# Performance work log

Hardware: AMD Instinct MI355X
Metric: run time of the kernel (lower is better)

The kernel has to match this reference:

```python
import jax, jax.numpy as jnp
import numpy as np

T, J, IC = 243, 17, 32
C = J * IC            # 544 embed dim
BS = 3                # block_size
NB = T // BS          # 81 num_blocks
K = 6                 # top_k
H = 8                 # num_heads
DEPTH = 2
HID = int(C * 2.0)    # 1088 mlp hidden
EPS = 1e-6


def _ln(x, g, b):
    m = x.mean(-1, keepdims=True)
    v = ((x - m) ** 2).mean(-1, keepdims=True)
    return (x - m) * jax.lax.rsqrt(v + EPS) * g + b


def setup_inputs() -> dict:
    key = jax.random.key(0)
    ks = jax.random.split(key, 16)
    s = 0.02
    B = 512
    return {
        "x": jax.random.normal(ks[0], (B, T, J, IC), jnp.float32),
        "pos_embed": s * jax.random.normal(ks[1], (1, T, C), jnp.float32),
        "fc1_w": s * jax.random.normal(ks[2], (NB, NB), jnp.float32),
        "fc2_w": s * jax.random.normal(ks[3], (NB, NB), jnp.float32),
        "ln1_g": jnp.ones((DEPTH, C), jnp.float32),
        "ln1_b": jnp.zeros((DEPTH, C), jnp.float32),
        "qkv_w": s * jax.random.normal(ks[4], (DEPTH, 3 * C, C), jnp.float32),
        "qkv_b": jnp.zeros((DEPTH, 3 * C), jnp.float32),
        "proj_w": s * jax.random.normal(ks[5], (DEPTH, C, C), jnp.float32),
        "proj_b": jnp.zeros((DEPTH, C), jnp.float32),
        "ln2_g": jnp.ones((DEPTH, C), jnp.float32),
        "ln2_b": jnp.zeros((DEPTH, C), jnp.float32),
        "mfc1_w": s * jax.random.normal(ks[6], (DEPTH, HID, C), jnp.float32),
        "mfc1_b": jnp.zeros((DEPTH, HID), jnp.float32),
        "mfc2_w": s * jax.random.normal(ks[7], (DEPTH, C, HID), jnp.float32),
        "mfc2_b": jnp.zeros((DEPTH, C), jnp.float32),
        "lnf_g": jnp.ones((C,), jnp.float32),
        "lnf_b": jnp.zeros((C,), jnp.float32),
        "wm2_w": s * jax.random.normal(ks[8], (K,), jnp.float32),
        "wm2_b": jnp.zeros((1,), jnp.float32),
    }


def reference(x, pos_embed, fc1_w, fc2_w, ln1_g, ln1_b, qkv_w, qkv_b,
              proj_w, proj_b, ln2_g, ln2_b, mfc1_w, mfc1_b, mfc2_w, mfc2_b,
              lnf_g, lnf_b, wm2_w, wm2_b):
    B = x.shape[0]
    x = x.reshape(B, T, C) + pos_embed                       # [B,T,C]
    # time_shift: zero-pad one frame at the front, keep first T rows, first C/2 chans
    shifted = jnp.pad(x, ((0, 0), (1, 0), (0, 0)))[:, :T, :C // 2]
    x = jnp.concatenate([shifted, x[:, :, C // 2:]], axis=2)
    # block pooling
    xb = x.reshape(B, NB, BS, C).mean(axis=2)                # [B,NB,C]
    # BlockAttention: global avg over C -> gated MLP -> topk -> gather
    y = xb.mean(axis=2)                                      # [B,NB]
    y = jax.nn.sigmoid(jnp.maximum(y @ fc1_w.T, 0.0) @ fc2_w.T)
    _, idx = jax.lax.top_k(y, K)                             # [B,K]
    t = jnp.take_along_axis(xb, idx[:, :, None], axis=1)     # [B,K,C]
    scale = (C // H) ** -0.5
    for i in range(DEPTH):
        h = _ln(t, ln1_g[i], ln1_b[i])
        qkv = (h @ qkv_w[i].T + qkv_b[i]).reshape(B, K, 3, H, C // H)
        q, k, v = qkv[:, :, 0], qkv[:, :, 1], qkv[:, :, 2]   # [B,K,H,hd]
        attn = jax.nn.softmax(jnp.einsum('bnhd,bmhd->bhnm', q, k) * scale, axis=-1)
        o = jnp.einsum('bhnm,bmhd->bnhd', attn, v).reshape(B, K, C)
        t = t + o @ proj_w[i].T + proj_b[i]
        h = _ln(t, ln2_g[i], ln2_b[i])
        h = jax.nn.gelu(h @ mfc1_w[i].T + mfc1_b[i], approximate=False)
        t = t + (h @ mfc2_w[i].T + mfc2_b[i])
    t = _ln(t, lnf_g, lnf_b)
    out = jnp.einsum('bkc,k->bc', t, wm2_w) + wm2_b          # Conv1d(K,1,ks=1)
    return out.reshape(B, 1, J, C // J)
```

## Files before the change

kernel.cpp:

```cpp
#include <hip/hip_runtime.h>
#include <hip/hip_bf16.h>
#include <math.h>

#define TT 243
#define CC 544
#define NBB 81
#define KK 6
#define HH 8
#define HD 68
#define DEPTH 2
#define HID 1088
#define BB 512
#define MTOK 3072
#define EPSF 1e-6f

typedef __attribute__((ext_vector_type(8))) short bf16x8;
typedef __attribute__((ext_vector_type(4))) float f32x4;

__device__ __forceinline__ __hip_bfloat16 f2b(float f) { return __float2bfloat16(f); }
__device__ __forceinline__ unsigned short f2bu(float f) {
    __hip_bfloat16 h = __float2bfloat16(f);
    return *(unsigned short*)&h;
}
__device__ __forceinline__ float b2f_lo(unsigned int u) { return __uint_as_float(u << 16); }
__device__ __forceinline__ float b2f_hi(unsigned int u) { return __uint_as_float(u & 0xffff0000u); }

#define E0 443904
#define E1 591872
#define E2 887808
#define E3 1183744

#define RS_BLOCKS 3888
#define PS_BLOCKS 8
#define WC_BLOCKS 4624
#define BW_GRID (RS_BLOCKS + PS_BLOCKS + WC_BLOCKS)

__global__ __launch_bounds__(256, 4) void bw_kernel(
    const float* __restrict__ x,
    const float* __restrict__ pos,
    const float* __restrict__ qkvw, const float* __restrict__ projw,
    const float* __restrict__ mfc1w, const float* __restrict__ mfc2w,
    unsigned short* __restrict__ wbf,
    float* __restrict__ L,
    float* __restrict__ R,
    float* __restrict__ pLR)
{
    const int blk = blockIdx.x;
    const int tid = threadIdx.x;

    if (blk < RS_BLOCKS) {
        const int w = tid >> 6;
        const int lane = tid & 63;
        const int oct = lane & 7;
        const int rsub = lane >> 3;
        const int r = (blk * 4 + w) * 8 + rsub;
        const float4* xr = (const float4*)x + (size_t)r * 136;
        float4 xs[17];
#pragma unroll
        for (int j = 0; j < 17; ++j) xs[j] = xr[oct + j * 8];
        float aL = 0.0f, aR = 0.0f;
#pragma unroll
        for (int j = 0; j < 17; ++j) {
            const float s = (xs[j].x + xs[j].y) + (xs[j].z + xs[j].w);
            if (j < 8) aL += s;
            else if (j == 8) { if (oct < 4) aL += s; else aR += s; }
            else aR += s;
        }
#pragma unroll
        for (int m = 1; m < 8; m <<= 1) {
            aL += __shfl_xor(aL, m);
            aR += __shfl_xor(aR, m);
        }
        if (oct == 0) { L[r] = aL; R[r] = aR; }
        return;
    }

    if (blk < RS_BLOCKS + PS_BLOCKS) {
        const int w = tid >> 6;
        const int lane = tid & 63;
        const int oct = lane & 7;
        const int rsub = lane >> 3;
        const int r = (blk - RS_BLOCKS) * 32 + w * 8 + rsub;
        const int rc = (r < TT) ? r : (TT - 1);
        const float4* pr = (const float4*)pos + (size_t)rc * 136;
        float4 xs[17];
#pragma unroll
        for (int j = 0; j < 17; ++j) xs[j] = pr[oct + j * 8];
        float aL = 0.0f, aR = 0.0f;
#pragma unroll
        for (int j = 0; j < 17; ++j) {
            const float s = (xs[j].x + xs[j].y) + (xs[j].z + xs[j].w);
            if (j < 8) aL += s;
            else if (j == 8) { if (oct < 4) aL += s; else aR += s; }
            else aR += s;
        }
#pragma unroll
        for (int m = 1; m < 8; m <<= 1) {
            aL += __shfl_xor(aL, m);
            aR += __shfl_xor(aR, m);
        }
        if (oct == 0 && r < TT) { pLR[r] = aL; pLR[TT + r] = aR; }
        return;
    }

    const int i = (blk - RS_BLOCKS - PS_BLOCKS) * 256 + tid;
    if (i < E3) {
        float4 v;
        if (i < E0)      v = ((const float4*)qkvw)[i];
        else if (i < E1) v = ((const float4*)projw)[i - E0];
        else if (i < E2) v = ((const float4*)mfc1w)[i - E1];
        else             v = ((const float4*)mfc2w)[i - E2];
        ushort4 o;
        o.x = f2bu(v.x); o.y = f2bu(v.y); o.z = f2bu(v.z); o.w = f2bu(v.w);
        ((ushort4*)wbf)[i] = o;
    }
}

__global__ __launch_bounds__(128) void select_kernel(
    const float* __restrict__ L, const float* __restrict__ R,
    const float* __restrict__ pLR,
    const float* __restrict__ fc1, const float* __restrict__ fc2,
    const float* __restrict__ x, const float* __restrict__ pos,
    const float* __restrict__ ln1g, const float* __restrict__ ln1b,
    float* __restrict__ t,
    unsigned short* __restrict__ hb)
{
    const int b = blockIdx.x;
    const int tid = threadIdx.x;
    __shared__ float sf1[NBB * NBB];
    __shared__ float sf2[NBB * NBB];
    __shared__ float sy[NBB], sz[NBB], swv[NBB];
    __shared__ int sidx[KK];
    __shared__ __align__(16) float st[KK][CC];

    const int w = tid >> 6;
    const int lane = tid & 63;
    const float4* x4 = (const float4*)x;
    const float4* p4 = (const float4*)pos;

    for (int i = tid; i < NBB * NBB; i += 128) {
        sf1[i] = fc1[i];
        sf2[i] = fc2[i];
    }

    if (tid < NBB) {
        const int n = tid;
        const float* Lb = L + (size_t)b * TT;
        const float* Rb = R + (size_t)b * TT;
        const float* pL = pLR;
        const float* pR = pLR + TT;
        float s = Lb[3 * n] + Lb[3 * n + 1] + Rb[3 * n] + Rb[3 * n + 1] + Rb[3 * n + 2]
                + pL[3 * n] + pL[3 * n + 1] + pR[3 * n] + pR[3 * n + 1] + pR[3 * n + 2];
        if (n > 0) s += Lb[3 * n - 1] + pL[3 * n - 1];
        sy[n] = s * (1.0f / (3.0f * (float)CC));
    }
    __syncthreads();
    if (tid < NBB) {
        float s = 0.0f;
        for (int j = 0; j < NBB; ++j) s += sf1[tid * NBB + j] * sy[j];
        sz[tid] = fmaxf(s, 0.0f);
    }
    __syncthreads();
    if (tid < NBB) {
        float s = 0.0f;
        for (int j = 0; j < NBB; ++j) s += sf2[tid * NBB + j] * sz[j];
        swv[tid] = 1.0f / (1.0f + expf(-s));
    }
    __syncthreads();
    if (w == 0) {
        float va = (lane < NBB) ? swv[lane] : -1e30f;
        float vb = (lane + 64 < NBB) ? swv[lane + 64] : -1e30f;
        const int ia = lane, ib = lane + 64;
        for (int kk = 0; kk < KK; ++kk) {
            float v = va; int idx = ia;
            if (vb > v) { v = vb; idx = ib; }
#pragma unroll
            for (int m = 1; m < 64; m <<= 1) {
                const float ov = __shfl_xor(v, m);
                const int oi = __shfl_xor(idx, m);
                if (ov > v || (ov == v && oi < idx)) { v = ov; idx = oi; }
            }
            if (lane == 0) sidx[kk] = idx;
            if (ia == idx) va = -1e30f;
            if (ib == idx) vb = -1e30f;
        }
    }
    __syncthreads();

    for (int i = tid; i < KK * 136; i += 128) {
        const int k = i / 136;
        const int c4 = i - k * 136;
        const int n = sidx[k];
        const int shift = (c4 < 68) ? -1 : 0;
        float ax = 0.f, ay = 0.f, az = 0.f, aw = 0.f;
#pragma unroll
        for (int i2 = 0; i2 < 3; ++i2) {
            const int ttr = 3 * n + i2 + shift;
            if (ttr >= 0) {
                const float4 xv = x4[((size_t)b * TT + ttr) * 136 + c4];
                const float4 pv = p4[(size_t)ttr * 136 + c4];
                ax += xv.x + pv.x; ay += xv.y + pv.y; az += xv.z + pv.z; aw += xv.w + pv.w;
            }
        }
        const float inv3 = 1.0f / 3.0f;
        const float4 a = make_float4(ax * inv3, ay * inv3, az * inv3, aw * inv3);
        *(float4*)&st[k][c4 * 4] = a;
        ((float4*)t)[((size_t)b * KK + k) * 136 + c4] = a;
    }
    __syncthreads();

    for (int k = w; k < KK; k += 2) {
        float s = 0.0f, s2 = 0.0f;
        for (int c = lane; c < CC; c += 64) { const float v = st[k][c]; s += v; s2 += v * v; }
#pragma unroll
        for (int off = 32; off; off >>= 1) {
            s += __shfl_xor(s, off);
            s2 += __shfl_xor(s2, off);
        }
        const float m = s / (float)CC;
        const float inv = rsqrtf(s2 / (float)CC - m * m + EPSF);
        for (int c4 = lane; c4 < 136; c4 += 64) {
            const float4 v = *(const float4*)&st[k][c4 * 4];
            const float4 gv = ((const float4*)ln1g)[c4];
            const float4 bv = ((const float4*)ln1b)[c4];
            ushort4 o;
            o.x = f2bu((v.x - m) * inv * gv.x + bv.x);
            o.y = f2bu((v.y - m) * inv * gv.y + bv.y);
            o.z = f2bu((v.z - m) * inv * gv.z + bv.z);
            o.w = f2bu((v.w - m) * inv * gv.w + bv.w);
            ((ushort4*)hb)[((size_t)b * KK + k) * 136 + c4] = o;
        }
    }
}

__global__ __launch_bounds__(256) void ln_bf16_kernel(
    const float* __restrict__ X, const float* __restrict__ g,
    const float* __restrict__ bta, unsigned short* __restrict__ Y)
{
    const int row = blockIdx.x * 4 + (threadIdx.x >> 6);
    const int lane = threadIdx.x & 63;
    const float4* xr4 = (const float4*)(X + (size_t)row * CC);
    const float4 v0 = xr4[lane];
    const float4 v1 = xr4[lane + 64];
    float4 v2 = make_float4(0.f, 0.f, 0.f, 0.f);
    if (lane < 8) v2 = xr4[lane + 128];
    float s = (v0.x + v0.y + v0.z + v0.w) + (v1.x + v1.y + v1.z + v1.w)
            + (v2.x + v2.y + v2.z + v2.w);
    float s2 = (v0.x * v0.x + v0.y * v0.y + v0.z * v0.z + v0.w * v0.w)
             + (v1.x * v1.x + v1.y * v1.y + v1.z * v1.z + v1.w * v1.w)
             + (v2.x * v2.x + v2.y * v2.y + v2.z * v2.z + v2.w * v2.w);
#pragma unroll
    for (int off = 32; off; off >>= 1) {
        s += __shfl_xor(s, off);
        s2 += __shfl_xor(s2, off);
    }
    const float m = s / (float)CC;
    const float inv = rsqrtf(s2 / (float)CC - m * m + EPSF);
    ushort4* yr = (ushort4*)(Y + (size_t)row * CC);
    {
        const float4 gv = ((const float4*)g)[lane];
        const float4 bv = ((const float4*)bta)[lane];
        ushort4 o;
        o.x = f2bu((v0.x - m) * inv * gv.x + bv.x);
        o.y = f2bu((v0.y - m) * inv * gv.y + bv.y);
        o.z = f2bu((v0.z - m) * inv * gv.z + bv.z);
        o.w = f2bu((v0.w - m) * inv * gv.w + bv.w);
        yr[lane] = o;
    }
    {
        const float4 gv = ((const float4*)g)[lane + 64];
        const float4 bv = ((const float4*)bta)[lane + 64];
        ushort4 o;
        o.x = f2bu((v1.x - m) * inv * gv.x + bv.x);
        o.y = f2bu((v1.y - m) * inv * gv.y + bv.y);
        o.z = f2bu((v1.z - m) * inv * gv.z + bv.z);
        o.w = f2bu((v1.w - m) * inv * gv.w + bv.w);
        yr[lane + 64] = o;
    }
    if (lane < 8) {
        const float4 gv = ((const float4*)g)[lane + 128];
        const float4 bv = ((const float4*)bta)[lane + 128];
        ushort4 o;
        o.x = f2bu((v2.x - m) * inv * gv.x + bv.x);
        o.y = f2bu((v2.y - m) * inv * gv.y + bv.y);
        o.z = f2bu((v2.z - m) * inv * gv.z + bv.z);
        o.w = f2bu((v2.w - m) * inv * gv.w + bv.w);
        yr[lane + 128] = o;
    }
}

template <int ACT, int RES, int OBF>
__global__ __launch_bounds__(256) void gemm_mfma_kernel(
    const unsigned short* __restrict__ X,
    const unsigned short* __restrict__ W,
    const float* __restrict__ bias,
    const float* __restrict__ Rr,
    void* __restrict__ Y,
    int M, int N, int Kd)
{
    const int bm = blockIdx.y * 128;
    const int bn = blockIdx.x * 128;
    const int tid = threadIdx.x;
    const int K8 = Kd >> 3;

    __shared__ __align__(16) short As[128][72];
    __shared__ __align__(16) short Bs[128][72];

    const int r0 = tid >> 2;
    const int c0 = tid & 3;
    const int r1 = r0 + 64;

    const uint4* Xu = (const uint4*)X;
    const uint4* Wu = (const uint4*)W;

    const int wid = tid >> 6;
    const int lane = tid & 63;
    const int wm = (wid >> 1) * 64;
    const int wn = (wid & 1) * 64;
    const int l16 = lane & 15;
    const int l4 = lane >> 4;
    const int koff = l4 * 8;

    f32x4 acc[4][4] = {};

    const int wr0 = min(bn + r0, N - 1);
    const int wr1 = min(bn + r1, N - 1);

    const uint4 zz = {0u, 0u, 0u, 0u};
    uint4 a00, a01, a10, a11, b00, b01, b10, b11;
    {
        const int k1 = c0, k2 = c0 + 4;
        a00 = (k1 < K8) ? Xu[(size_t)(bm + r0) * K8 + k1] : zz;
        a01 = (k2 < K8) ? Xu[(size_t)(bm + r0) * K8 + k2] : zz;
        a10 = (k1 < K8) ? Xu[(size_t)(bm + r1) * K8 + k1] : zz;
        a11 = (k2 < K8) ? Xu[(size_t)(bm + r1) * K8 + k2] : zz;
        b00 = (k1 < K8) ? Wu[(size_t)wr0 * K8 + k1] : zz;
        b01 = (k2 < K8) ? Wu[(size_t)wr0 * K8 + k2] : zz;
        b10 = (k1 < K8) ? Wu[(size_t)wr1 * K8 + k1] : zz;
        b11 = (k2 < K8) ? Wu[(size_t)wr1 * K8 + k2] : zz;
    }

    const int nk = (Kd + 63) >> 6;
    for (int kt = 0; kt < nk; ++kt) {
        __syncthreads();
        *(uint4*)&As[r0][c0 * 8]       = a00;
        *(uint4*)&As[r0][(c0 + 4) * 8] = a01;
        *(uint4*)&As[r1][c0 * 8]       = a10;
        *(uint4*)&As[r1][(c0 + 4) * 8] = a11;
        *(uint4*)&Bs[r0][c0 * 8]       = b00;
        *(uint4*)&Bs[r0][(c0 + 4) * 8] = b01;
        *(uint4*)&Bs[r1][c0 * 8]       = b10;
        *(uint4*)&Bs[r1][(c0 + 4) * 8] = b11;
        __syncthreads();

        if (kt + 1 < nk) {
            const int k1 = (kt + 1) * 8 + c0;
            const int k2 = k1 + 4;
            a00 = (k1 < K8) ? Xu[(size_t)(bm + r0) * K8 + k1] : zz;
            a01 = (k2 < K8) ? Xu[(size_t)(bm + r0) * K8 + k2] : zz;
            a10 = (k1 < K8) ? Xu[(size_t)(bm + r1) * K8 + k1] : zz;
            a11 = (k2 < K8) ? Xu[(size_t)(bm + r1) * K8 + k2] : zz;
            b00 = (k1 < K8) ? Wu[(size_t)wr0 * K8 + k1] : zz;
            b01 = (k2 < K8) ? Wu[(size_t)wr0 * K8 + k2] : zz;
            b10 = (k1 < K8) ? Wu[(size_t)wr1 * K8 + k1] : zz;
            b11 = (k2 < K8) ? Wu[(size_t)wr1 * K8 + k2] : zz;
        }

#pragma unroll
        for (int kh = 0; kh < 2; ++kh) {
            bf16x8 af[4], bf[4];
#pragma unroll
            for (int mf = 0; mf < 4; ++mf)
                af[mf] = *(const bf16x8*)&As[wm + mf * 16 + l16][kh * 32 + koff];
#pragma unroll
            for (int nf = 0; nf < 4; ++nf)
                bf[nf] = *(const bf16x8*)&Bs[wn + nf * 16 + l16][kh * 32 + koff];
#pragma unroll
            for (int mf = 0; mf < 4; ++mf)
#pragma unroll
                for (int nf = 0; nf < 4; ++nf)
                    acc[mf][nf] = __builtin_amdgcn_mfma_f32_16x16x32_bf16(af[mf], bf[nf], acc[mf][nf], 0, 0, 0);
        }
    }

#pragma unroll
    for (int nf = 0; nf < 4; ++nf) {
        const int col = bn + wn + nf * 16 + l16;
        if (col < N) {
            const float bs = bias[col];
#pragma unroll
            for (int mf = 0; mf < 4; ++mf) {
#pragma unroll
                for (int j = 0; j < 4; ++j) {
                    const int row = bm + wm + mf * 16 + l4 * 4 + j;
                    float v = acc[mf][nf][j] + bs;
                    if (ACT == 1) v = 0.5f * v * (1.0f + erff(v * 0.70710678118654752f));
                    if (RES) v += Rr[(size_t)row * N + col];
                    if (OBF) ((unsigned short*)Y)[(size_t)row * N + col] = f2bu(v);
                    else     ((float*)Y)[(size_t)row * N + col] = v;
                }
            }
        }
    }
}

__global__ __launch_bounds__(512) void attn_kernel(
    const unsigned short* __restrict__ qkv,
    __hip_bfloat16* __restrict__ o)
{
    const int b = blockIdx.x;
    __shared__ __align__(16) float sq[KK * 3 * CC];
    __shared__ float sp[HH][40];
    const int tid = threadIdx.x;

    const uint4* src4 = (const uint4*)(qkv + (size_t)b * KK * 3 * CC);
    for (int i = tid; i < (KK * 3 * CC) / 8; i += 512) {
        const uint4 u = src4[i];
        float4 f0, f1;
        f0.x = b2f_lo(u.x); f0.y = b2f_hi(u.x);
        f0.z = b2f_lo(u.y); f0.w = b2f_hi(u.y);
        f1.x = b2f_lo(u.z); f1.y = b2f_hi(u.z);
        f1.z = b2f_lo(u.w); f1.w = b2f_hi(u.w);
        ((float4*)sq)[2 * i] = f0;
        ((float4*)sq)[2 * i + 1] = f1;
    }
    __syncthreads();

    const int h = tid >> 6;
    const int lane = tid & 63;
    const float scl = rsqrtf((float)HD);

    if (lane < KK * KK) {
        const int n = lane / KK, m = lane - (lane / KK) * KK;
        const float* qp = &sq[n * (3 * CC) + 0 * CC + h * HD];
        const float* kp = &sq[m * (3 * CC) + 1 * CC + h * HD];
        float s = 0.0f;
#pragma unroll 4
        for (int d = 0; d < HD; ++d) s += qp[d] * kp[d];
        sp[h][lane] = s * scl;
    }
    __syncthreads();
    if (lane < KK) {
        const int n = lane;
        float mx = -1e30f;
#pragma unroll
        for (int m = 0; m < KK; ++m) mx = fmaxf(mx, sp[h][n * KK + m]);
        float e[KK];
        float sum = 0.0f;
#pragma unroll
        for (int m = 0; m < KK; ++m) { e[m] = expf(sp[h][n * KK + m] - mx); sum += e[m]; }
        const float inv = 1.0f / sum;
#pragma unroll
        for (int m = 0; m < KK; ++m) sp[h][n * KK + m] = e[m] * inv;
    }
    __syncthreads();
    for (int i = tid; i < KK * CC; i += 512) {
        const int n = i / CC;
        const int cd = i - n * CC;
        const int hh = cd / HD;
        const int d = cd - hh * HD;
        float acc = 0.0f;
#pragma unroll
        for (int m = 0; m < KK; ++m)
            acc += sp[hh][n * KK + m] * sq[m * (3 * CC) + 2 * CC + hh * HD + d];
        o[(size_t)b * KK * CC + i] = f2b(acc);
    }
}

__global__ __launch_bounds__(256) void final_kernel(
    const float* __restrict__ t, const float* __restrict__ g,
    const float* __restrict__ bta, const float* __restrict__ wm2w,
    const float* __restrict__ wm2b, float* __restrict__ out)
{
    const int b = blockIdx.x;
    const int tid = threadIdx.x;
    __shared__ float st[KK][CC];
    __shared__ float sm[KK], si[KK];
    const float* tb = t + (size_t)b * KK * CC;
    for (int i = tid; i < KK * CC; i += 256) st[i / CC][i % CC] = tb[i];
    __syncthreads();
    const int wid = tid >> 6, lane = tid & 63;
    for (int r = wid; r < KK; r += 4) {
        float s = 0.0f, s2 = 0.0f;
        for (int c = lane; c < CC; c += 64) { const float v = st[r][c]; s += v; s2 += v * v; }
#pragma unroll
        for (int off = 32; off; off >>= 1) { s += __shfl_xor(s, off); s2 += __shfl_xor(s2, off); }
        if (lane == 0) {
            const float m = s / (float)CC;
            sm[r] = m;
            si[r] = rsqrtf(s2 / (float)CC - m * m + EPSF);
        }
    }
    __syncthreads();
    const float w0 = wm2w[0], w1 = wm2w[1], w2 = wm2w[2], w3 = wm2w[3], w4 = wm2w[4], w5 = wm2w[5];
    const float wb = wm2b[0];
    for (int c = tid; c < CC; c += 256) {
        const float gg = g[c], bb = bta[c];
        float acc = wb;
        acc += w0 * ((st[0][c] - sm[0]) * si[0] * gg + bb);
        acc += w1 * ((st[1][c] - sm[1]) * si[1] * gg + bb);
        acc += w2 * ((st[2][c] - sm[2]) * si[2] * gg + bb);
        acc += w3 * ((st[3][c] - sm[3]) * si[3] * gg + bb);
        acc += w4 * ((st[4][c] - sm[4]) * si[4] * gg + bb);
        acc += w5 * ((st[5][c] - sm[5]) * si[5] * gg + bb);
        out[(size_t)b * CC + c] = acc;
    }
}

extern "C" void kernel_launch(void* const* d_in, const int* in_sizes, int n_in,
                              void* d_out, int out_size, void* d_ws, size_t ws_size,
                              hipStream_t stream)
{
    const float* x      = (const float*)d_in[0];
    const float* pos    = (const float*)d_in[1];
    const float* fc1_w  = (const float*)d_in[2];
    const float* fc2_w  = (const float*)d_in[3];
    const float* ln1_g  = (const float*)d_in[4];
    const float* ln1_b  = (const float*)d_in[5];
    const float* qkv_w  = (const float*)d_in[6];
    const float* qkv_b  = (const float*)d_in[7];
    const float* proj_w = (const float*)d_in[8];
    const float* proj_b = (const float*)d_in[9];
    const float* ln2_g  = (const float*)d_in[10];
    const float* ln2_b  = (const float*)d_in[11];
    const float* mfc1_w = (const float*)d_in[12];
    const float* mfc1_b = (const float*)d_in[13];
    const float* mfc2_w = (const float*)d_in[14];
    const float* mfc2_b = (const float*)d_in[15];
    const float* lnf_g  = (const float*)d_in[16];
    const float* lnf_b  = (const float*)d_in[17];
    const float* wm2_w  = (const float*)d_in[18];
    const float* wm2_b  = (const float*)d_in[19];

    float* ws = (float*)d_ws;
    float* L    = ws;
    float* R    = L + 124416;
    float* pLR  = R + 124416;
    float* t    = pLR + 512;
    unsigned short* qkvb = (unsigned short*)(t + (size_t)MTOK * CC);
    unsigned short* hb  = qkvb + (size_t)MTOK * 3 * CC;
    unsigned short* ob  = hb + (size_t)MTOK * CC;
    unsigned short* gb  = ob + (size_t)MTOK * CC;
    unsigned short* wbf = gb + (size_t)MTOK * HID;

    unsigned short* wqkv = wbf;
    unsigned short* wprj = wbf + 1775616;
    unsigned short* wf1  = wbf + 2367488;
    unsigned short* wf2  = wbf + 3551232;

    bw_kernel<<<BW_GRID, 256, 0, stream>>>(
        x, pos, qkv_w, proj_w, mfc1_w, mfc2_w, wbf, L, R, pLR);

    select_kernel<<<BB, 128, 0, stream>>>(
        L, R, pLR, fc1_w, fc2_w, x, pos, ln1_g, ln1_b, t, hb);

    for (int i = 0; i < DEPTH; ++i) {
        if (i > 0) {
            ln_bf16_kernel<<<MTOK / 4, 256, 0, stream>>>(t, ln1_g + i * CC, ln1_b + i * CC, hb);
        }
        gemm_mfma_kernel<0, 0, 1><<<dim3(13, 24), 256, 0, stream>>>(
            hb, wqkv + (size_t)i * 1632 * 544, qkv_b + (size_t)i * 3 * CC,
            nullptr, qkvb, MTOK, 3 * CC, CC);
        attn_kernel<<<BB, 512, 0, stream>>>(qkvb, (__hip_bfloat16*)ob);
        gemm_mfma_kernel<0, 1, 0><<<dim3(5, 24), 256, 0, stream>>>(
            ob, wprj + (size_t)i * 544 * 544, proj_b + (size_t)i * CC,
            t, t, MTOK, CC, CC);
        ln_bf16_kernel<<<MTOK / 4, 256, 0, stream>>>(t, ln2_g + i * CC, ln2_b + i * CC, hb);
        gemm_mfma_kernel<1, 0, 1><<<dim3(9, 24), 256, 0, stream>>>(
            hb, wf1 + (size_t)i * HID * 544, mfc1_b + (size_t)i * HID,
            nullptr, gb, MTOK, HID, CC);
        gemm_mfma_kernel<0, 1, 0><<<dim3(5, 24), 256, 0, stream>>>(
            gb, wf2 + (size_t)i * 544 * HID, mfc2_b + (size_t)i * CC,
            t, t, MTOK, CC, HID);
    }

    final_kernel<<<BB, 256, 0, stream>>>(t, lnf_g, lnf_b, wm2_w, wm2_b, (float*)d_out);
}
```

Before: 253.2 us.

## Fuse LayerNorm into GEMMs via per-row partial statistics from residual epilogues

```diff
diff --git a/kernel.cpp b/kernel.cpp
--- a/kernel.cpp
+++ b/kernel.cpp
@@ -13,6 +13,7 @@
 #define BB 512
 #define MTOK 3072
 #define EPSF 1e-6f
+#define NPART 10
 
 typedef __attribute__((ext_vector_type(8))) short bf16x8;
 typedef __attribute__((ext_vector_type(4))) float f32x4;
@@ -25,6 +26,16 @@
 __device__ __forceinline__ float b2f_lo(unsigned int u) { return __uint_as_float(u << 16); }
 __device__ __forceinline__ float b2f_hi(unsigned int u) { return __uint_as_float(u & 0xffff0000u); }
 
+__device__ __forceinline__ ushort4 norm4(float4 f, float m, float inv,
+                                         const float* sg, const float* sb, int c) {
+    ushort4 o;
+    o.x = f2bu((f.x - m) * inv * sg[c + 0] + sb[c + 0]);
+    o.y = f2bu((f.y - m) * inv * sg[c + 1] + sb[c + 1]);
+    o.z = f2bu((f.z - m) * inv * sg[c + 2] + sb[c + 2]);
+    o.w = f2bu((f.w - m) * inv * sg[c + 3] + sb[c + 3]);
+    return o;
+}
+
 #define E0 443904
 #define E1 591872
 #define E2 887808
@@ -36,14 +47,11 @@
 #define BW_GRID (RS_BLOCKS + PS_BLOCKS + WC_BLOCKS)
 
 __global__ __launch_bounds__(256, 4) void bw_kernel(
-    const float* __restrict__ x,
-    const float* __restrict__ pos,
+    const float* __restrict__ x, const float* __restrict__ pos,
     const float* __restrict__ qkvw, const float* __restrict__ projw,
     const float* __restrict__ mfc1w, const float* __restrict__ mfc2w,
     unsigned short* __restrict__ wbf,
-    float* __restrict__ L,
-    float* __restrict__ R,
-    float* __restrict__ pLR)
+    float* __restrict__ L, float* __restrict__ R, float* __restrict__ pLR)
 {
     const int blk = blockIdx.x;
     const int tid = threadIdx.x;
@@ -122,8 +130,7 @@
     const float* __restrict__ fc1, const float* __restrict__ fc2,
     const float* __restrict__ x, const float* __restrict__ pos,
     const float* __restrict__ ln1g, const float* __restrict__ ln1b,
-    float* __restrict__ t,
-    unsigned short* __restrict__ hb)
+    float* __restrict__ t, unsigned short* __restrict__ hb)
 {
     const int b = blockIdx.x;
     const int tid = threadIdx.x;
@@ -233,68 +240,16 @@
     }
 }
 
-__global__ __launch_bounds__(256) void ln_bf16_kernel(
-    const float* __restrict__ X, const float* __restrict__ g,
-    const float* __restrict__ bta, unsigned short* __restrict__ Y)
-{
-    const int row = blockIdx.x * 4 + (threadIdx.x >> 6);
-    const int lane = threadIdx.x & 63;
-    const float4* xr4 = (const float4*)(X + (size_t)row * CC);
-    const float4 v0 = xr4[lane];
-    const float4 v1 = xr4[lane + 64];
-    float4 v2 = make_float4(0.f, 0.f, 0.f, 0.f);
-    if (lane < 8) v2 = xr4[lane + 128];
-    float s = (v0.x + v0.y + v0.z + v0.w) + (v1.x + v1.y + v1.z + v1.w)
-            + (v2.x + v2.y + v2.z + v2.w);
-    float s2 = (v0.x * v0.x + v0.y * v0.y + v0.z * v0.z + v0.w * v0.w)
-             + (v1.x * v1.x + v1.y * v1.y + v1.z * v1.z + v1.w * v1.w)
-             + (v2.x * v2.x + v2.y * v2.y + v2.z * v2.z + v2.w * v2.w);
-#pragma unroll
-    for (int off = 32; off; off >>= 1) {
-        s += __shfl_xor(s, off);
-        s2 += __shfl_xor(s2, off);
-    }
-    const float m = s / (float)CC;
-    const float inv = rsqrtf(s2 / (float)CC - m * m + EPSF);
-    ushort4* yr = (ushort4*)(Y + (size_t)row * CC);
-    {
-        const float4 gv = ((const float4*)g)[lane];
-        const float4 bv = ((const float4*)bta)[lane];
-        ushort4 o;
-        o.x = f2bu((v0.x - m) * inv * gv.x + bv.x);
-        o.y = f2bu((v0.y - m) * inv * gv.y + bv.y);
-        o.z = f2bu((v0.z - m) * inv * gv.z + bv.z);
-        o.w = f2bu((v0.w - m) * inv * gv.w + bv.w);
-        yr[lane] = o;
-    }
-    {
-        const float4 gv = ((const float4*)g)[lane + 64];
-        const float4 bv = ((const float4*)bta)[lane + 64];
-        ushort4 o;
-        o.x = f2bu((v1.x - m) * inv * gv.x + bv.x);
-        o.y = f2bu((v1.y - m) * inv * gv.y + bv.y);
-        o.z = f2bu((v1.z - m) * inv * gv.z + bv.z);
-        o.w = f2bu((v1.w - m) * inv * gv.w + bv.w);
-        yr[lane + 64] = o;
-    }
-    if (lane < 8) {
-        const float4 gv = ((const float4*)g)[lane + 128];
-        const float4 bv = ((const float4*)bta)[lane + 128];
-        ushort4 o;
-        o.x = f2bu((v2.x - m) * inv * gv.x + bv.x);
-        o.y = f2bu((v2.y - m) * inv * gv.y + bv.y);
-        o.z = f2bu((v2.z - m) * inv * gv.z + bv.z);
-        o.w = f2bu((v2.w - m) * inv * gv.w + bv.w);
-        yr[lane + 128] = o;
-    }
-}
-
-template <int ACT, int RES, int OBF>
+template <int LNS, int ACT, int RES, int STATS, int OBF>
 __global__ __launch_bounds__(256) void gemm_mfma_kernel(
-    const unsigned short* __restrict__ X,
+    const void* __restrict__ Xv,
     const unsigned short* __restrict__ W,
     const float* __restrict__ bias,
     const float* __restrict__ Rr,
+    const float* __restrict__ lng,
+    const float* __restrict__ lnb,
+    const float* __restrict__ Sin,
+    float* __restrict__ Sout,
     void* __restrict__ Y,
     int M, int N, int Kd)
 {
@@ -302,17 +257,19 @@
     const int bn = blockIdx.x * 128;
     const int tid = threadIdx.x;
     const int K8 = Kd >> 3;
+    const int K4 = Kd >> 2;
 
     __shared__ __align__(16) short As[128][72];
     __shared__ __align__(16) short Bs[128][72];
+    __shared__ __align__(16) float sgb[LNS ? 2 * CC + 256 : 1];
+    float* sg = sgb;
+    float* sb = sgb + CC;
+    float* smean_l = sgb + 2 * CC;
+    float* sinv_l = sgb + 2 * CC + 128;
 
     const int r0 = tid >> 2;
     const int c0 = tid & 3;
     const int r1 = r0 + 64;
-
-    const uint4* Xu = (const uint4*)X;
-    const uint4* Wu = (const uint4*)W;
-
     const int wid = tid >> 6;
     const int lane = tid & 63;
     const int wm = (wid >> 1) * 64;
@@ -321,19 +278,59 @@
     const int l4 = lane >> 4;
     const int koff = l4 * 8;
 
+    if constexpr (LNS) {
+        for (int i = tid; i < 136; i += 256) {
+            ((float4*)sg)[i] = ((const float4*)lng)[i];
+            ((float4*)sb)[i] = ((const float4*)lnb)[i];
+        }
+        if (tid < 128) {
+            const int row = bm + tid;
+            float s = 0.f, s2 = 0.f;
+#pragma unroll
+            for (int p = 0; p < NPART; ++p) {
+                s += Sin[(size_t)p * (MTOK * 2) + row * 2];
+                s2 += Sin[(size_t)p * (MTOK * 2) + row * 2 + 1];
+            }
+            const float mm = s / (float)CC;
+            smean_l[tid] = mm;
+            sinv_l[tid] = rsqrtf(s2 / (float)CC - mm * mm + EPSF);
+        }
+        __syncthreads();
+    }
+
     f32x4 acc[4][4] = {};
 
+    const uint4* Wu = (const uint4*)W;
     const int wr0 = min(bn + r0, N - 1);
     const int wr1 = min(bn + r1, N - 1);
 
     const uint4 zz = {0u, 0u, 0u, 0u};
-    uint4 a00, a01, a10, a11, b00, b01, b10, b11;
+    const float4 fz = make_float4(0.f, 0.f, 0.f, 0.f);
+
+    uint4 a00, a01, a10, a11;
+    float4 fA[8];
+    uint4 b00, b01, b10, b11;
     {
         const int k1 = c0, k2 = c0 + 4;
-        a00 = (k1 < K8) ? Xu[(size_t)(bm + r0) * K8 + k1] : zz;
-        a01 = (k2 < K8) ? Xu[(size_t)(bm + r0) * K8 + k2] : zz;
-        a10 = (k1 < K8) ? Xu[(size_t)(bm + r1) * K8 + k1] : zz;
-        a11 = (k2 < K8) ? Xu[(size_t)(bm + r1) * K8 + k2] : zz;
+        if constexpr (LNS) {
+            const float4* Xf = (const float4*)Xv;
+            const size_t ro0 = (size_t)(bm + r0) * K4;
+            const size_t ro1 = (size_t)(bm + r1) * K4;
+            fA[0] = (k1 < K8) ? Xf[ro0 + 2 * k1] : fz;
+            fA[1] = (k1 < K8) ? Xf[ro0 + 2 * k1 + 1] : fz;
+            fA[2] = (k2 < K8) ? Xf[ro0 + 2 * k2] : fz;
+            fA[3] = (k2 < K8) ? Xf[ro0 + 2 * k2 + 1] : fz;
+            fA[4] = (k1 < K8) ? Xf[ro1 + 2 * k1] : fz;
+            fA[5] = (k1 < K8) ? Xf[ro1 + 2 * k1 + 1] : fz;
+            fA[6] = (k2 < K8) ? Xf[ro1 + 2 * k2] : fz;
+            fA[7] = (k2 < K8) ? Xf[ro1 + 2 * k2 + 1] : fz;
+        } else {
+            const uint4* Xu = (const uint4*)Xv;
+            a00 = (k1 < K8) ? Xu[(size_t)(bm + r0) * K8 + k1] : zz;
+            a01 = (k2 < K8) ? Xu[(size_t)(bm + r0) * K8 + k2] : zz;
+            a10 = (k1 < K8) ? Xu[(size_t)(bm + r1) * K8 + k1] : zz;
+            a11 = (k2 < K8) ? Xu[(size_t)(bm + r1) * K8 + k2] : zz;
+        }
         b00 = (k1 < K8) ? Wu[(size_t)wr0 * K8 + k1] : zz;
         b01 = (k2 < K8) ? Wu[(size_t)wr0 * K8 + k2] : zz;
         b10 = (k1 < K8) ? Wu[(size_t)wr1 * K8 + k1] : zz;
@@ -343,10 +340,28 @@
     const int nk = (Kd + 63) >> 6;
     for (int kt = 0; kt < nk; ++kt) {
         __syncthreads();
-        *(uint4*)&As[r0][c0 * 8]       = a00;
-        *(uint4*)&As[r0][(c0 + 4) * 8] = a01;
-        *(uint4*)&As[r1][c0 * 8]       = a10;
-        *(uint4*)&As[r1][(c0 + 4) * 8] = a11;
+        if constexpr (LNS) {
+            const bool w1 = (kt * 8 + c0) < K8;
+            const bool w2 = (kt * 8 + c0 + 4) < K8;
+            const float m0 = smean_l[r0], i0 = sinv_l[r0];
+            const float m1 = smean_l[r1], i1 = sinv_l[r1];
+            const int cb1 = kt * 64 + c0 * 8;
+            const int cb2 = cb1 + 32;
+            const ushort4 z4 = {0, 0, 0, 0};
+            *(ushort4*)&As[r0][c0 * 8]           = w1 ? norm4(fA[0], m0, i0, sg, sb, cb1) : z4;
+            *(ushort4*)&As[r0][c0 * 8 + 4]       = w1 ? norm4(fA[1], m0, i0, sg, sb, cb1 + 4) : z4;
+            *(ushort4*)&As[r0][(c0 + 4) * 8]     = w2 ? norm4(fA[2], m0, i0, sg, sb, cb2) : z4;
+            *(ushort4*)&As[r0][(c0 + 4) * 8 + 4] = w2 ? norm4(fA[3], m0, i0, sg, sb, cb2 + 4) : z4;
+            *(ushort4*)&As[r1][c0 * 8]           = w1 ? norm4(fA[4], m1, i1, sg, sb, cb1) : z4;
+            *(ushort4*)&As[r1][c0 * 8 + 4]       = w1 ? norm4(fA[5], m1, i1, sg, sb, cb1 + 4) : z4;
+            *(ushort4*)&As[r1][(c0 + 4) * 8]     = w2 ? norm4(fA[6], m1, i1, sg, sb, cb2) : z4;
+            *(ushort4*)&As[r1][(c0 + 4) * 8 + 4] = w2 ? norm4(fA[7], m1, i1, sg, sb, cb2 + 4) : z4;
+        } else {
+            *(uint4*)&As[r0][c0 * 8]       = a00;
+            *(uint4*)&As[r0][(c0 + 4) * 8] = a01;
+            *(uint4*)&As[r1][c0 * 8]       = a10;
+            *(uint4*)&As[r1][(c0 + 4) * 8] = a11;
+        }
         *(uint4*)&Bs[r0][c0 * 8]       = b00;
         *(uint4*)&Bs[r0][(c0 + 4) * 8] = b01;
         *(uint4*)&Bs[r1][c0 * 8]       = b10;
@@ -356,10 +371,25 @@
         if (kt + 1 < nk) {
             const int k1 = (kt + 1) * 8 + c0;
             const int k2 = k1 + 4;
-            a00 = (k1 < K8) ? Xu[(size_t)(bm + r0) * K8 + k1] : zz;
-            a01 = (k2 < K8) ? Xu[(size_t)(bm + r0) * K8 + k2] : zz;
-            a10 = (k1 < K8) ? Xu[(size_t)(bm + r1) * K8 + k1] : zz;
-            a11 = (k2 < K8) ? Xu[(size_t)(bm + r1) * K8 + k2] : zz;
+            if constexpr (LNS) {
+                const float4* Xf = (const float4*)Xv;
+                const size_t ro0 = (size_t)(bm + r0) * K4;
+                const size_t ro1 = (size_t)(bm + r1) * K4;
+                fA[0] = (k1 < K8) ? Xf[ro0 + 2 * k1] : fz;
+                fA[1] = (k1 < K8) ? Xf[ro0 + 2 * k1 + 1] : fz;
+                fA[2] = (k2 < K8) ? Xf[ro0 + 2 * k2] : fz;
+                fA[3] = (k2 < K8) ? Xf[ro0 + 2 * k2 + 1] : fz;
+                fA[4] = (k1 < K8) ? Xf[ro1 + 2 * k1] : fz;
+                fA[5] = (k1 < K8) ? Xf[ro1 + 2 * k1 + 1] : fz;
+                fA[6] = (k2 < K8) ? Xf[ro1 + 2 * k2] : fz;
+                fA[7] = (k2 < K8) ? Xf[ro1 + 2 * k2 + 1] : fz;
+            } else {
+                const uint4* Xu = (const uint4*)Xv;
+                a00 = (k1 < K8) ? Xu[(size_t)(bm + r0) * K8 + k1] : zz;
+                a01 = (k2 < K8) ? Xu[(size_t)(bm + r0) * K8 + k2] : zz;
+                a10 = (k1 < K8) ? Xu[(size_t)(bm + r1) * K8 + k1] : zz;
+                a11 = (k2 < K8) ? Xu[(size_t)(bm + r1) * K8 + k2] : zz;
+            }
             b00 = (k1 < K8) ? Wu[(size_t)wr0 * K8 + k1] : zz;
             b01 = (k2 < K8) ? Wu[(size_t)wr0 * K8 + k2] : zz;
             b10 = (k1 < K8) ? Wu[(size_t)wr1 * K8 + k1] : zz;
@@ -383,22 +413,52 @@
         }
     }
 
+    float ssum[16], ssq[16];
+    if constexpr (STATS) {
+#pragma unroll
+        for (int q = 0; q < 16; ++q) { ssum[q] = 0.f; ssq[q] = 0.f; }
+    }
+
 #pragma unroll
     for (int nf = 0; nf < 4; ++nf) {
         const int col = bn + wn + nf * 16 + l16;
-        if (col < N) {
-            const float bs = bias[col];
-#pragma unroll
-            for (int mf = 0; mf < 4; ++mf) {
-#pragma unroll
-                for (int j = 0; j < 4; ++j) {
-                    const int row = bm + wm + mf * 16 + l4 * 4 + j;
-                    float v = acc[mf][nf][j] + bs;
-                    if (ACT == 1) v = 0.5f * v * (1.0f + erff(v * 0.70710678118654752f));
+        const bool ok = col < N;
+        const float bs = ok ? bias[col] : 0.0f;
+#pragma unroll
+        for (int mf = 0; mf < 4; ++mf) {
+#pragma unroll
+            for (int j = 0; j < 4; ++j) {
+                const int row = bm + wm + mf * 16 + l4 * 4 + j;
+                float v = acc[mf][nf][j] + bs;
+                if (ACT == 1) v = 0.5f * v * (1.0f + erff(v * 0.70710678118654752f));
+                if (ok) {
                     if (RES) v += Rr[(size_t)row * N + col];
                     if (OBF) ((unsigned short*)Y)[(size_t)row * N + col] = f2bu(v);
                     else     ((float*)Y)[(size_t)row * N + col] = v;
+                    if constexpr (STATS) {
+                        ssum[mf * 4 + j] += v;
+                        ssq[mf * 4 + j] += v * v;
+                    }
                 }
+            }
+        }
+    }
+
+    if constexpr (STATS) {
+#pragma unroll
+        for (int q = 0; q < 16; ++q) {
+            float a = ssum[q], bq = ssq[q];
+#pragma unroll
+            for (int m = 1; m < 16; m <<= 1) {
+                a += __shfl_xor(a, m);
+                bq += __shfl_xor(bq, m);
+            }
+            if (l16 == 0) {
+                const int row_l = wm + (q >> 2) * 16 + l4 * 4 + (q & 3);
+                const int p = ((bn >> 7) * 2) + (wn >> 6);
+                float* dst = Sout + (size_t)p * (MTOK * 2) + (size_t)(bm + row_l) * 2;
+                dst[0] = a;
+                dst[1] = bq;
             }
         }
     }
@@ -470,7 +530,8 @@
 __global__ __launch_bounds__(256) void final_kernel(
     const float* __restrict__ t, const float* __restrict__ g,
     const float* __restrict__ bta, const float* __restrict__ wm2w,
-    const float* __restrict__ wm2b, float* __restrict__ out)
+    const float* __restrict__ wm2b, const float* __restrict__ Sin,
+    float* __restrict__ out)
 {
     const int b = blockIdx.x;
     const int tid = threadIdx.x;
@@ -478,18 +539,17 @@
     __shared__ float sm[KK], si[KK];
     const float* tb = t + (size_t)b * KK * CC;
     for (int i = tid; i < KK * CC; i += 256) st[i / CC][i % CC] = tb[i];
-    __syncthreads();
-    const int wid = tid >> 6, lane = tid & 63;
-    for (int r = wid; r < KK; r += 4) {
-        float s = 0.0f, s2 = 0.0f;
-        for (int c = lane; c < CC; c += 64) { const float v = st[r][c]; s += v; s2 += v * v; }
-#pragma unroll
-        for (int off = 32; off; off >>= 1) { s += __shfl_xor(s, off); s2 += __shfl_xor(s2, off); }
-        if (lane == 0) {
-            const float m = s / (float)CC;
-            sm[r] = m;
-            si[r] = rsqrtf(s2 / (float)CC - m * m + EPSF);
-        }
+    if (tid < KK) {
+        const int row = b * KK + tid;
+        float s = 0.f, s2 = 0.f;
+#pragma unroll
+        for (int p = 0; p < NPART; ++p) {
+            s += Sin[(size_t)p * (MTOK * 2) + row * 2];
+            s2 += Sin[(size_t)p * (MTOK * 2) + row * 2 + 1];
+        }
+        const float m = s / (float)CC;
+        sm[tid] = m;
+        si[tid] = rsqrtf(s2 / (float)CC - m * m + EPSF);
     }
     __syncthreads();
     const float w0 = wm2w[0], w1 = wm2w[1], w2 = wm2w[2], w3 = wm2w[3], w4 = wm2w[4], w5 = wm2w[5];
@@ -536,7 +596,11 @@
     float* L    = ws;
     float* R    = L + 124416;
     float* pLR  = R + 124416;
-    float* t    = pLR + 512;
+    float* S1   = pLR + 512;
+    float* S2   = S1 + NPART * MTOK * 2;
+    float* S3   = S2 + NPART * MTOK * 2;
+    float* S4   = S3 + NPART * MTOK * 2;
+    float* t    = S4 + NPART * MTOK * 2;
     unsigned short* qkvb = (unsigned short*)(t + (size_t)MTOK * CC);
     unsigned short* hb  = qkvb + (size_t)MTOK * 3 * CC;
     unsigned short* ob  = hb + (size_t)MTOK * CC;
@@ -554,25 +618,31 @@
     select_kernel<<<BB, 128, 0, stream>>>(
         L, R, pLR, fc1_w, fc2_w, x, pos, ln1_g, ln1_b, t, hb);
 
+    float* Sln2[2] = {S1, S3};
+    float* Sln1n[2] = {S2, S4};
     for (int i = 0; i < DEPTH; ++i) {
-        if (i > 0) {
-            ln_bf16_kernel<<<MTOK / 4, 256, 0, stream>>>(t, ln1_g + i * CC, ln1_b + i * CC, hb);
-        }
-        gemm_mfma_kernel<0, 0, 1><<<dim3(13, 24), 256, 0, stream>>>(
-            hb, wqkv + (size_t)i * 1632 * 544, qkv_b + (size_t)i * 3 * CC,
-            nullptr, qkvb, MTOK, 3 * CC, CC);
+        if (i == 0) {
+            gemm_mfma_kernel<0, 0, 0, 0, 1><<<dim3(13, 24), 256, 0, stream>>>(
+                hb, wqkv, qkv_b, nullptr, nullptr, nullptr, nullptr, nullptr,
+                qkvb, MTOK, 3 * CC, CC);
+        } else {
+            gemm_mfma_kernel<1, 0, 0, 0, 1><<<dim3(13, 24), 256, 0, stream>>>(
+                t, wqkv + (size_t)i * 1632 * 544, qkv_b + (size_t)i * 3 * CC,
+                nullptr, ln1_g + i * CC, ln1_b + i * CC, Sln1n[0], nullptr,
+                qkvb, MTOK, 3 * CC, CC);
+        }
         attn_kernel<<<BB, 512, 0, stream>>>(qkvb, (__hip_bfloat16*)ob);
-        gemm_mfma_kernel<0, 1, 0><<<dim3(5, 24), 256, 0, stream>>>(
+        gemm_mfma_kernel<0, 0, 1, 1, 0><<<dim3(5, 24), 256, 0, stream>>>(
             ob, wprj + (size_t)i * 544 * 544, proj_b + (size_t)i * CC,
-            t, t, MTOK, CC, CC);
-        ln_bf16_kernel<<<MTOK / 4, 256, 0, stream>>>(t, ln2_g + i * CC, ln2_b + i * CC, hb);
-        gemm_mfma_kernel<1, 0, 1><<<dim3(9, 24), 256, 0, stream>>>(
-            hb, wf1 + (size_t)i * HID * 544, mfc1_b + (size_t)i * HID,
-            nullptr, gb, MTOK, HID, CC);
-        gemm_mfma_kernel<0, 1, 0><<<dim3(5, 24), 256, 0, stream>>>(
+            t, nullptr, nullptr, nullptr, Sln2[i], t, MTOK, CC, CC);
+        gemm_mfma_kernel<1, 1, 0, 0, 1><<<dim3(9, 24), 256, 0, stream>>>(
+            t, wf1 + (size_t)i * HID * 544, mfc1_b + (size_t)i * HID,
+            nullptr, ln2_g + i * CC, ln2_b + i * CC, Sln2[i], nullptr,
+            gb, MTOK, HID, CC);
+        gemm_mfma_kernel<0, 0, 1, 1, 0><<<dim3(5, 24), 256, 0, stream>>>(
             gb, wf2 + (size_t)i * 544 * HID, mfc2_b + (size_t)i * CC,
-            t, t, MTOK, CC, HID);
-    }
-
-    final_kernel<<<BB, 256, 0, stream>>>(t, lnf_g, lnf_b, wm2_w, wm2_b, (float*)d_out);
-}
+            t, nullptr, nullptr, nullptr, Sln1n[i], t, MTOK, CC, HID);
+    }
+
+    final_kernel<<<BB, 256, 0, stream>>>(t, lnf_g, lnf_b, wm2_w, wm2_b, S4, (float*)d_out);
+}
```

New measurement: 427.9 us. 69.0% more time.
